# Kernel tuning notes

Measured on AMD Instinct MI355X. Metric: run time of the kernel, lower is better.

The kernel has to match this reference:

```python
import jax, jax.numpy as jnp
import numpy as np

B, L, H, T = 128, 256, 1024, 9


def setup_inputs() -> dict:
    key = jax.random.key(0)
    ks = jax.random.split(key, 7)
    hidden = jax.random.normal(ks[0], (B, L, H), dtype=jnp.float32)
    W = jax.random.normal(ks[1], (T, H), dtype=jnp.float32) * 0.02  # nn.Linear weight (T, H)
    b = jnp.zeros((T,), dtype=jnp.float32)
    start_transitions = jax.random.normal(ks[2], (T,), dtype=jnp.float32) * 0.1
    end_transitions = jax.random.normal(ks[3], (T,), dtype=jnp.float32) * 0.1
    transitions = jax.random.normal(ks[4], (T, T), dtype=jnp.float32) * 0.1
    labels = jax.random.randint(ks[5], (B, L), 0, T, dtype=jnp.int32)
    lengths = jax.random.randint(ks[6], (B,), 1, L + 1, dtype=jnp.int32)
    return dict(hidden=hidden, W=W, b=b, start_transitions=start_transitions,
                end_transitions=end_transitions, transitions=transitions,
                labels=labels, lengths=lengths)


def _crf_nll(emissions, tags, mask, start_t, end_t, trans):
    """pytorch-crf forward(): mean log-likelihood, negated.
    emissions: (B,L,T) float; tags: (B,L) int; mask: (B,L) bool with mask[:,0]=True.
    """
    Bsz = emissions.shape[0]
    maskf = mask.astype(emissions.dtype)
    bar = jnp.arange(Bsz)
    # ---- numerator: score of the gold path ----
    t0 = tags[:, 0]
    num = start_t[t0] + emissions[bar, 0, t0]
    prev, cur = tags[:, :-1], tags[:, 1:]
    em_tag = jnp.take_along_axis(emissions[:, 1:, :], cur[:, :, None], axis=2)[:, :, 0]
    num = num + jnp.sum((trans[prev, cur] + em_tag) * maskf[:, 1:], axis=1)
    seq_ends = jnp.sum(mask.astype(jnp.int32), axis=1) - 1
    last_tags = tags[bar, seq_ends]
    num = num + end_t[last_tags]
    # ---- denominator: log-partition via forward algorithm (lax.scan over time) ----
    score0 = start_t[None, :] + emissions[:, 0, :]                 # (B,T)
    em_rest = jnp.transpose(emissions[:, 1:, :], (1, 0, 2))        # (L-1,B,T)
    m_rest = jnp.transpose(mask[:, 1:], (1, 0))                    # (L-1,B)

    def step(score, xs):
        em_t, m_t = xs
        nxt = jax.nn.logsumexp(score[:, :, None] + trans[None, :, :] + em_t[:, None, :], axis=1)
        return jnp.where(m_t[:, None], nxt, score), None

    score, _ = jax.lax.scan(step, score0, (em_rest, m_rest))
    denom = jax.nn.logsumexp(score + end_t[None, :], axis=1)
    llh = num - denom
    return -jnp.mean(llh)  # reduction='mean', loss = -log_likelihood


def reference(hidden, W, b, start_transitions, end_transitions, transitions, labels, lengths):
    # dropout is identity in eval; classifier linear -> emissions
    emissions = jnp.einsum('blh,th->blt', hidden, W) + b
    mask = jnp.arange(L)[None, :] < lengths[:, None]
    mask = mask.at[:, 0].set(True)  # crf_mask[:, 0] = True
    return _crf_nll(emissions, labels, mask, start_transitions, end_transitions, transitions)
```

## Files before the change

kernel.cpp:

```cpp
#include <hip/hip_runtime.h>
#include <math.h>

#define Bn 128
#define Ln 256
#define Hn 1024
#define Tn 9

__device__ __forceinline__ float dot4(float4 a, float4 b) {
  return a.x*b.x + a.y*b.y + a.z*b.z + a.w*b.w;
}

__global__ __launch_bounds__(256, 2) void emis_kernel(
    const float* __restrict__ hidden, const float* __restrict__ W,
    const float* __restrict__ bias, float* __restrict__ em)
{
  const int lane = threadIdx.x & 63;
  const int wid  = blockIdx.x * (blockDim.x >> 6) + (threadIdx.x >> 6);
  const int nw   = gridDim.x * (blockDim.x >> 6);

  const float4* W4 = (const float4*)W;
  float4 w[9][4];
#pragma unroll
  for (int t = 0; t < 9; ++t)
#pragma unroll
    for (int j = 0; j < 4; ++j)
      w[t][j] = W4[t*256 + j*64 + lane];

  const int NROWS = Bn * Ln;
  int row = wid;
  if (row >= NROWS) return;

  const float4* hp = (const float4*)hidden + (size_t)row * 256 + lane;
  float4 h0 = hp[0], h1 = hp[64], h2 = hp[128], h3 = hp[192];

  while (true) {
    const int nrow = row + nw;
    float4 n0, n1, n2, n3;
    if (nrow < NROWS) {
      const float4* hq = (const float4*)hidden + (size_t)nrow * 256 + lane;
      n0 = hq[0]; n1 = hq[64]; n2 = hq[128]; n3 = hq[192];
    }

    float acc[9];
#pragma unroll
    for (int t = 0; t < 9; ++t)
      acc[t] = dot4(h0, w[t][0]) + dot4(h1, w[t][1])
             + dot4(h2, w[t][2]) + dot4(h3, w[t][3]);

#pragma unroll
    for (int t = 0; t < 9; ++t) {
#pragma unroll
      for (int m = 1; m < 64; m <<= 1)
        acc[t] += __shfl_xor(acc[t], m, 64);
    }

    float v = acc[0];
#pragma unroll
    for (int t = 1; t < 9; ++t)
      if (lane == t) v = acc[t];
    if (lane < 9) em[(size_t)row * 9 + lane] = v + bias[lane];

    if (nrow >= NROWS) break;
    row = nrow; h0 = n0; h1 = n1; h2 = n2; h3 = n3;
  }
}

__global__ __launch_bounds__(64) void crf_kernel(
    const float* __restrict__ em, const int* __restrict__ labels,
    const int* __restrict__ lengths, const float* __restrict__ start_t,
    const float* __restrict__ end_t, const float* __restrict__ trans,
    float* __restrict__ llh)
{
  const int b    = blockIdx.x;
  const int lane = threadIdx.x;
  const int len  = lengths[b];
  const float* emb = em + (size_t)b * Ln * Tn;
  const int*   tg  = labels + b * Ln;

  float part = 0.f;
  for (int t = lane; t < len; t += 64) {
    const int cur = tg[t];
    float v;
    if (t == 0) v = start_t[cur] + emb[cur];
    else        v = trans[tg[t-1] * Tn + cur] + emb[t * Tn + cur];
    if (t == len - 1) v += end_t[cur];
    part += v;
  }
#pragma unroll
  for (int m = 1; m < 64; m <<= 1) part += __shfl_xor(part, m, 64);
  const float num = part;

  const int j = (lane < Tn) ? lane : 0;
  float trc[9];
#pragma unroll
  for (int i = 0; i < 9; ++i) trc[i] = trans[i * Tn + j];

  float score = start_t[j] + emb[j];
  for (int t = 1; t < len; ++t) {
    const float e = emb[t * Tn + j];
    float a[9];
#pragma unroll
    for (int i = 0; i < 9; ++i) a[i] = __shfl(score, i, 64) + trc[i];
    float mx = a[0];
#pragma unroll
    for (int i = 1; i < 9; ++i) mx = fmaxf(mx, a[i]);
    float s = 0.f;
#pragma unroll
    for (int i = 0; i < 9; ++i) s += __expf(a[i] - mx);
    score = mx + __logf(s) + e;
  }

  float fin = (lane < Tn) ? (score + end_t[j]) : -1.0e30f;
  float mx = fin;
#pragma unroll
  for (int m = 1; m < 64; m <<= 1) mx = fmaxf(mx, __shfl_xor(mx, m, 64));
  float se = __expf(fin - mx);
#pragma unroll
  for (int m = 1; m < 64; m <<= 1) se += __shfl_xor(se, m, 64);
  const float denom = mx + __logf(se);

  if (lane == 0) llh[b] = num - denom;
}

__global__ __launch_bounds__(64) void reduce_kernel(
    const float* __restrict__ llh, float* __restrict__ out)
{
  const int lane = threadIdx.x;
  float v = llh[lane] + llh[lane + 64];
#pragma unroll
  for (int m = 1; m < 64; m <<= 1) v += __shfl_xor(v, m, 64);
  if (lane == 0) out[0] = -v * (1.0f / Bn);
}

extern "C" void kernel_launch(void* const* d_in, const int* in_sizes, int n_in,
                              void* d_out, int out_size, void* d_ws, size_t ws_size,
                              hipStream_t stream) {
  const float* hidden  = (const float*)d_in[0];
  const float* W       = (const float*)d_in[1];
  const float* bias    = (const float*)d_in[2];
  const float* start_t = (const float*)d_in[3];
  const float* end_t   = (const float*)d_in[4];
  const float* trans   = (const float*)d_in[5];
  const int*   labels  = (const int*)d_in[6];
  const int*   lengths = (const int*)d_in[7];

  float* out = (float*)d_out;
  float* em  = (float*)d_ws;
  float* llh = em + (size_t)Bn * Ln * Tn;

  emis_kernel<<<512, 256, 0, stream>>>(hidden, W, bias, em);
  crf_kernel<<<Bn, 64, 0, stream>>>(em, labels, lengths, start_t, end_t, trans, llh);
  reduce_kernel<<<1, 64, 0, stream>>>(llh, out);
}
```

Measured before the change: 260.3 us.

## Use bf16 MFMA for emissions and chunk-parallel CRF forward via transfer matrices

Emission projection is rewritten to convert hidden and W to bf16 and use 16x16x32 MFMA with K split over four waves, writing partial sums that a new combine kernel adds together with the bias. The sequential CRF forward recursion is split into 8 chunks of 32 steps. One block per (batch, chunk, start state) computes a 9x9 log-space transfer matrix, and a second kernel chains the 8 matrices. This removes the long serial 256-step dependency and the FP32 dot-product bottleneck, at the cost of bf16 precision loss, extra launches and extra workspace traffic.

```diff
diff --git a/kernel.cpp b/kernel.cpp
--- a/kernel.cpp
+++ b/kernel.cpp
@@ -5,84 +5,137 @@
 #define Ln 256
 #define Hn 1024
 #define Tn 9
-
-__device__ __forceinline__ float dot4(float4 a, float4 b) {
-  return a.x*b.x + a.y*b.y + a.z*b.z + a.w*b.w;
-}
-
-__global__ __launch_bounds__(256, 2) void emis_kernel(
+#define NROWS (Bn * Ln)
+#define NTILE (NROWS / 16)
+#define EMN   (NROWS * Tn)
+
+typedef short short8 __attribute__((ext_vector_type(8)));
+typedef float f32x4  __attribute__((ext_vector_type(4)));
+typedef int   i32x4  __attribute__((ext_vector_type(4)));
+
+__device__ __forceinline__ unsigned cvt_pk_bf16(float a, float b) {
+  unsigned r;
+  asm("v_cvt_pk_bf16_f32 %0, %1, %2" : "=v"(r) : "v"(a), "v"(b));
+  return r;
+}
+
+__device__ __forceinline__ short8 pack_bf16x8(float4 lo, float4 hi) {
+  i32x4 u;
+  u[0] = cvt_pk_bf16(lo.x, lo.y);
+  u[1] = cvt_pk_bf16(lo.z, lo.w);
+  u[2] = cvt_pk_bf16(hi.x, hi.y);
+  u[3] = cvt_pk_bf16(hi.z, hi.w);
+  return __builtin_bit_cast(short8, u);
+}
+
+__global__ __launch_bounds__(256, 4) void emis_mfma_kernel(
     const float* __restrict__ hidden, const float* __restrict__ W,
-    const float* __restrict__ bias, float* __restrict__ em)
+    float* __restrict__ part)
 {
   const int lane = threadIdx.x & 63;
-  const int wid  = blockIdx.x * (blockDim.x >> 6) + (threadIdx.x >> 6);
-  const int nw   = gridDim.x * (blockDim.x >> 6);
-
-  const float4* W4 = (const float4*)W;
-  float4 w[9][4];
-#pragma unroll
-  for (int t = 0; t < 9; ++t)
-#pragma unroll
-    for (int j = 0; j < 4; ++j)
-      w[t][j] = W4[t*256 + j*64 + lane];
-
-  const int NROWS = Bn * Ln;
-  int row = wid;
-  if (row >= NROWS) return;
-
-  const float4* hp = (const float4*)hidden + (size_t)row * 256 + lane;
-  float4 h0 = hp[0], h1 = hp[64], h2 = hp[128], h3 = hp[192];
-
-  while (true) {
-    const int nrow = row + nw;
-    float4 n0, n1, n2, n3;
-    if (nrow < NROWS) {
-      const float4* hq = (const float4*)hidden + (size_t)nrow * 256 + lane;
-      n0 = hq[0]; n1 = hq[64]; n2 = hq[128]; n3 = hq[192];
+  const int wid  = blockIdx.x * 4 + (threadIdx.x >> 6);
+  const int s    = wid & 3;
+  const int tile = wid >> 2;
+  const int col  = lane & 15;
+  const int g    = lane >> 4;
+
+  short8 bfrag[8];
+  if (col < Tn) {
+    const float* wr = W + col * Hn + s * 256 + g * 8;
+#pragma unroll
+    for (int m = 0; m < 8; ++m) {
+      float4 lo = *(const float4*)(wr + m * 32);
+      float4 hi = *(const float4*)(wr + m * 32 + 4);
+      bfrag[m] = pack_bf16x8(lo, hi);
     }
-
-    float acc[9];
-#pragma unroll
-    for (int t = 0; t < 9; ++t)
-      acc[t] = dot4(h0, w[t][0]) + dot4(h1, w[t][1])
-             + dot4(h2, w[t][2]) + dot4(h3, w[t][3]);
-
-#pragma unroll
-    for (int t = 0; t < 9; ++t) {
-#pragma unroll
-      for (int m = 1; m < 64; m <<= 1)
-        acc[t] += __shfl_xor(acc[t], m, 64);
-    }
-
-    float v = acc[0];
-#pragma unroll
-    for (int t = 1; t < 9; ++t)
-      if (lane == t) v = acc[t];
-    if (lane < 9) em[(size_t)row * 9 + lane] = v + bias[lane];
-
-    if (nrow >= NROWS) break;
-    row = nrow; h0 = n0; h1 = n1; h2 = n2; h3 = n3;
-  }
-}
-
-__global__ __launch_bounds__(64) void crf_kernel(
+  } else {
+#pragma unroll
+    for (int m = 0; m < 8; ++m) bfrag[m] = (short8)0;
+  }
+
+  const float* A = hidden + (size_t)tile * 16 * Hn + (size_t)col * Hn + s * 256 + g * 8;
+  float4 lo[8], hi[8];
+#pragma unroll
+  for (int m = 0; m < 8; ++m) {
+    lo[m] = *(const float4*)(A + m * 32);
+    hi[m] = *(const float4*)(A + m * 32 + 4);
+  }
+  f32x4 acc = {0.f, 0.f, 0.f, 0.f};
+#pragma unroll
+  for (int m = 0; m < 8; ++m) {
+    short8 af = pack_bf16x8(lo[m], hi[m]);
+    acc = __builtin_amdgcn_mfma_f32_16x16x32_bf16(af, bfrag[m], acc, 0, 0, 0);
+  }
+
+  if (col < Tn) {
+    float* p = part + (size_t)s * EMN;
+    const int rbase = tile * 16 + g * 4;
+#pragma unroll
+    for (int r = 0; r < 4; ++r)
+      p[(size_t)(rbase + r) * Tn + col] = acc[r];
+  }
+}
+
+__global__ __launch_bounds__(256) void combine_kernel(
+    const float* __restrict__ part, const float* __restrict__ bias,
+    float* __restrict__ em)
+{
+  const int i = blockIdx.x * 256 + threadIdx.x;
+  float v = part[i] + part[i + EMN] + part[i + 2 * EMN] + part[i + 3 * EMN];
+  em[i] = v + bias[i % Tn];
+}
+
+__global__ __launch_bounds__(64) void crfA_kernel(
+    const float* __restrict__ em, const int* __restrict__ lengths,
+    const float* __restrict__ trans, float* __restrict__ M)
+{
+  const int bid = blockIdx.x;
+  const int b = bid / 72, rem = bid % 72, c = rem / 9, s0 = rem % 9;
+  const int lane = threadIdx.x;
+  const int j = (lane < Tn) ? lane : 0;
+  const int len = lengths[b];
+  int lo = c * 32; if (lo < 1) lo = 1;
+  int hi = c * 32 + 32; if (hi > len) hi = len;
+
+  float trc[9];
+#pragma unroll
+  for (int i = 0; i < 9; ++i) trc[i] = trans[i * Tn + j];
+
+  float score = (j == s0) ? 0.f : -1.0e30f;
+  const float* emb = em + (size_t)b * Ln * Tn;
+  for (int t = lo; t < hi; ++t) {
+    const float e = emb[t * Tn + j];
+    float a[9];
+#pragma unroll
+    for (int i = 0; i < 9; ++i) a[i] = __shfl(score, i, 64) + trc[i];
+    float mx = a[0];
+#pragma unroll
+    for (int i = 1; i < 9; ++i) mx = fmaxf(mx, a[i]);
+    float ssum = 0.f;
+#pragma unroll
+    for (int i = 0; i < 9; ++i) ssum += __expf(a[i] - mx);
+    score = mx + __logf(ssum) + e;
+  }
+  if (lane < Tn)
+    M[((size_t)(b * 8 + c) * 9 + s0) * 9 + lane] = score;
+}
+
+__global__ __launch_bounds__(64) void crfB_kernel(
     const float* __restrict__ em, const int* __restrict__ labels,
     const int* __restrict__ lengths, const float* __restrict__ start_t,
     const float* __restrict__ end_t, const float* __restrict__ trans,
-    float* __restrict__ llh)
-{
-  const int b    = blockIdx.x;
-  const int lane = threadIdx.x;
-  const int len  = lengths[b];
+    const float* __restrict__ M, float* __restrict__ llh)
+{
+  const int b = blockIdx.x, lane = threadIdx.x;
+  const int len = lengths[b];
   const float* emb = em + (size_t)b * Ln * Tn;
-  const int*   tg  = labels + b * Ln;
+  const int* tg = labels + b * Ln;
 
   float part = 0.f;
   for (int t = lane; t < len; t += 64) {
     const int cur = tg[t];
-    float v;
-    if (t == 0) v = start_t[cur] + emb[cur];
-    else        v = trans[tg[t-1] * Tn + cur] + emb[t * Tn + cur];
+    float v = (t == 0) ? (start_t[cur] + emb[cur])
+                       : (trans[tg[t - 1] * Tn + cur] + emb[t * Tn + cur]);
     if (t == len - 1) v += end_t[cur];
     part += v;
   }
@@ -91,26 +144,22 @@
   const float num = part;
 
   const int j = (lane < Tn) ? lane : 0;
-  float trc[9];
-#pragma unroll
-  for (int i = 0; i < 9; ++i) trc[i] = trans[i * Tn + j];
-
-  float score = start_t[j] + emb[j];
-  for (int t = 1; t < len; ++t) {
-    const float e = emb[t * Tn + j];
+  float v = start_t[j] + emb[j];
+#pragma unroll
+  for (int c = 0; c < 8; ++c) {
+    const float* Mc = M + (size_t)(b * 8 + c) * 81;
     float a[9];
 #pragma unroll
-    for (int i = 0; i < 9; ++i) a[i] = __shfl(score, i, 64) + trc[i];
+    for (int i = 0; i < 9; ++i) a[i] = __shfl(v, i, 64) + Mc[i * 9 + j];
     float mx = a[0];
 #pragma unroll
     for (int i = 1; i < 9; ++i) mx = fmaxf(mx, a[i]);
-    float s = 0.f;
-#pragma unroll
-    for (int i = 0; i < 9; ++i) s += __expf(a[i] - mx);
-    score = mx + __logf(s) + e;
-  }
-
-  float fin = (lane < Tn) ? (score + end_t[j]) : -1.0e30f;
+    float ssum = 0.f;
+#pragma unroll
+    for (int i = 0; i < 9; ++i) ssum += __expf(a[i] - mx);
+    v = mx + __logf(ssum);
+  }
+  float fin = (lane < Tn) ? (v + end_t[j]) : -1.0e30f;
   float mx = fin;
 #pragma unroll
   for (int m = 1; m < 64; m <<= 1) mx = fmaxf(mx, __shfl_xor(mx, m, 64));
@@ -118,7 +167,6 @@
 #pragma unroll
   for (int m = 1; m < 64; m <<= 1) se += __shfl_xor(se, m, 64);
   const float denom = mx + __logf(se);
-
   if (lane == 0) llh[b] = num - denom;
 }
 
@@ -144,11 +192,16 @@
   const int*   labels  = (const int*)d_in[6];
   const int*   lengths = (const int*)d_in[7];
 
-  float* out = (float*)d_out;
-  float* em  = (float*)d_ws;
-  float* llh = em + (size_t)Bn * Ln * Tn;
-
-  emis_kernel<<<512, 256, 0, stream>>>(hidden, W, bias, em);
-  crf_kernel<<<Bn, 64, 0, stream>>>(em, labels, lengths, start_t, end_t, trans, llh);
+  float* out  = (float*)d_out;
+  float* wsf  = (float*)d_ws;
+  float* part = wsf;
+  float* em   = part + 4 * (size_t)EMN;
+  float* M    = em + (size_t)EMN;
+  float* llh  = M + (size_t)Bn * 8 * 81;
+
+  emis_mfma_kernel<<<NTILE, 256, 0, stream>>>(hidden, W, part);
+  combine_kernel<<<EMN / 256, 256, 0, stream>>>(part, bias, em);
+  crfA_kernel<<<Bn * 8 * 9, 64, 0, stream>>>(em, lengths, trans, M);
+  crfB_kernel<<<Bn, 64, 0, stream>>>(em, labels, lengths, start_t, end_t, trans, M, llh);
   reduce_kernel<<<1, 64, 0, stream>>>(llh, out);
 }
```

Measured after the change: 246.3 us. -5.4%, faster.
